# Kernel optimization log

Hardware: AMD Instinct MI355X
Metric: run time of the kernel (lower is better)

Reference implementation:

```python
import jax, jax.numpy as jnp
import numpy as np

B, N, D = 2, 2048, 1024   # batch, seq_len, d_model
E = 2 * D                  # d_inner = d_model * expand_factor
F = 4 * D                  # ffn hidden
CHUNK = 128
EPS_LN = 1e-5


def setup_inputs() -> dict:
    key = jax.random.key(0)
    ks = jax.random.split(key, 16)
    s = 0.02
    return {
        "x": jax.random.normal(ks[0], (B, N, D), dtype=jnp.float32),
        # linear-attention projections (stored [in, out])
        "q_w": jax.random.normal(ks[1], (D, E), dtype=jnp.float32) * s,
        "q_b": jnp.zeros((E,), jnp.float32),
        "k_w": jax.random.normal(ks[2], (D, E), dtype=jnp.float32) * s,
        "k_b": jnp.zeros((E,), jnp.float32),
        "v_w": jax.random.normal(ks[3], (D, E), dtype=jnp.float32) * s,
        "v_b": jnp.zeros((E,), jnp.float32),
        "o_w": jax.random.normal(ks[4], (E, D), dtype=jnp.float32) * s,
        "o_b": jnp.zeros((D,), jnp.float32),
        # layer norms
        "ln1_g": jnp.ones((D,), jnp.float32), "ln1_b": jnp.zeros((D,), jnp.float32),
        "ln2_g": jnp.ones((D,), jnp.float32), "ln2_b": jnp.zeros((D,), jnp.float32),
        # ffn
        "w1": jax.random.normal(ks[5], (D, F), dtype=jnp.float32) * s,
        "b1": jnp.zeros((F,), jnp.float32),
        "w2": jax.random.normal(ks[6], (F, D), dtype=jnp.float32) * s,
        "b2": jnp.zeros((D,), jnp.float32),
    }


def _layer_norm(x, g, b):
    mu = jnp.mean(x, axis=-1, keepdims=True)
    var = jnp.mean(jnp.square(x - mu), axis=-1, keepdims=True)
    return (x - mu) * jax.lax.rsqrt(var + EPS_LN) * g + b


def _feature_map(x):
    return jax.nn.elu(x) + 1.0  # positive features


def _causal_linear_attention(Q, K, V):
    """Exactly cumsum(k v^T) formulation, computed chunk-recurrently.
    Q,K: [B,N,E] (post feature map), V: [B,N,E]. Returns [B,N,E]."""
    nC = N // CHUNK
    Qc = Q.reshape(B, nC, CHUNK, E).transpose(1, 0, 2, 3)
    Kc = K.reshape(B, nC, CHUNK, E).transpose(1, 0, 2, 3)
    Vc = V.reshape(B, nC, CHUNK, E).transpose(1, 0, 2, 3)
    tril = jnp.tril(jnp.ones((CHUNK, CHUNK), Q.dtype))

    def step(S, qkv):  # S: [B,E,E] running sum of k v^T
        q, k, v = qkv
        scores = jnp.einsum('bcd,bkd->bck', q, k) * tril  # intra-chunk causal
        intra = jnp.einsum('bck,bke->bce', scores, v)
        inter = jnp.einsum('bcd,bde->bce', q, S)
        S = S + jnp.einsum('bcd,bce->bde', k, v)
        return S, intra + inter

    S0 = jnp.zeros((B, E, E), Q.dtype)
    _, num = jax.lax.scan(step, S0, (Qc, Kc, Vc))  # [nC,B,CHUNK,E]
    num = num.transpose(1, 0, 2, 3).reshape(B, N, E)
    Z = jnp.cumsum(K, axis=1)                       # [B,N,E]
    den = jnp.einsum('bnd,bnd->bn', Q, Z)[..., None] + 1e-6
    return num / den


def reference(x, q_w, q_b, k_w, k_b, v_w, v_b, o_w, o_b,
              ln1_g, ln1_b, ln2_g, ln2_b, w1, b1, w2, b2):
    # training branch of SSDFLUIDLayer (linear attention), dropout = identity (eval)
    xn = _layer_norm(x, ln1_g, ln1_b)
    Q = _feature_map(xn @ q_w + q_b)
    K = _feature_map(xn @ k_w + k_b)
    V = xn @ v_w + v_b
    attn = _causal_linear_attention(Q, K, V) @ o_w + o_b
    x = x + attn
    xn2 = _layer_norm(x, ln2_g, ln2_b)
    ffn = jax.nn.gelu(xn2 @ w1 + b1, approximate=False) @ w2 + b2
    return x + ffn
```

## Files before the change

kernel.cpp:

```cpp
#include <hip/hip_runtime.h>
#include <math.h>

typedef unsigned short u16;
typedef short s16x8 __attribute__((ext_vector_type(8)));
typedef float f32x4 __attribute__((ext_vector_type(4)));
typedef long long ll;

__device__ inline u16 f2bf(float f) {
    unsigned u = __float_as_uint(f);
    u += 0x7fffu + ((u >> 16) & 1u);
    return (u16)(u >> 16);
}
__device__ inline float bf2f(u16 h) { return __uint_as_float(((unsigned)h) << 16); }

__device__ __forceinline__ void glds16(const u16* g, u16* l) {
    __builtin_amdgcn_global_load_lds(
        (__attribute__((address_space(1))) void*)(void*)g,
        (__attribute__((address_space(3))) void*)l, 16, 0, 0);
}

__global__ __launch_bounds__(256) void ln_bf16(const float* __restrict__ x,
                                               const float* __restrict__ g,
                                               const float* __restrict__ b,
                                               u16* __restrict__ out, int D) {
    int row = blockIdx.x;
    const float* xr = x + (size_t)row * D;
    int t = threadIdx.x;
    float4 v = ((const float4*)xr)[t];
    float s = v.x + v.y + v.z + v.w;
    __shared__ float sm[4];
    #pragma unroll
    for (int o = 32; o > 0; o >>= 1) s += __shfl_down(s, o, 64);
    int lane = t & 63, wv = t >> 6;
    if (lane == 0) sm[wv] = s;
    __syncthreads();
    float mean = (sm[0] + sm[1] + sm[2] + sm[3]) * (1.0f / 1024.0f);
    float dx = v.x - mean, dy = v.y - mean, dz = v.z - mean, dw = v.w - mean;
    float s2 = dx * dx + dy * dy + dz * dz + dw * dw;
    __syncthreads();
    #pragma unroll
    for (int o = 32; o > 0; o >>= 1) s2 += __shfl_down(s2, o, 64);
    if (lane == 0) sm[wv] = s2;
    __syncthreads();
    float var = (sm[0] + sm[1] + sm[2] + sm[3]) * (1.0f / 1024.0f);
    float rstd = rsqrtf(var + 1e-5f);
    float4 gg = ((const float4*)g)[t], bb = ((const float4*)b)[t];
    ushort4 o4;
    o4.x = f2bf(dx * rstd * gg.x + bb.x);
    o4.y = f2bf(dy * rstd * gg.y + bb.y);
    o4.z = f2bf(dz * rstd * gg.z + bb.z);
    o4.w = f2bf(dw * rstd * gg.w + bb.w);
    ((ushort4*)(out + (size_t)row * D))[t] = o4;
}

__global__ __launch_bounds__(256) void combine_ln(
    const float* __restrict__ x, const float* __restrict__ p0,
    const float* __restrict__ p1, const float* __restrict__ ob,
    const float* __restrict__ g, const float* __restrict__ b,
    float* __restrict__ x2, u16* __restrict__ xn2) {
    int row = blockIdx.x;
    int t = threadIdx.x;
    size_t base = (size_t)row * 256;
    float4 v = ((const float4*)x)[base + t];
    float4 a0 = ((const float4*)p0)[base + t];
    float4 a1 = ((const float4*)p1)[base + t];
    float4 ob4 = ((const float4*)ob)[t];
    v.x += a0.x + a1.x + ob4.x;
    v.y += a0.y + a1.y + ob4.y;
    v.z += a0.z + a1.z + ob4.z;
    v.w += a0.w + a1.w + ob4.w;
    ((float4*)x2)[base + t] = v;
    float s = v.x + v.y + v.z + v.w;
    __shared__ float sm[4];
    #pragma unroll
    for (int o = 32; o > 0; o >>= 1) s += __shfl_down(s, o, 64);
    int lane = t & 63, wv = t >> 6;
    if (lane == 0) sm[wv] = s;
    __syncthreads();
    float mean = (sm[0] + sm[1] + sm[2] + sm[3]) * (1.0f / 1024.0f);
    float dx = v.x - mean, dy = v.y - mean, dz = v.z - mean, dw = v.w - mean;
    float s2 = dx * dx + dy * dy + dz * dz + dw * dw;
    __syncthreads();
    #pragma unroll
    for (int o = 32; o > 0; o >>= 1) s2 += __shfl_down(s2, o, 64);
    if (lane == 0) sm[wv] = s2;
    __syncthreads();
    float var = (sm[0] + sm[1] + sm[2] + sm[3]) * (1.0f / 1024.0f);
    float rstd = rsqrtf(var + 1e-5f);
    float4 gg = ((const float4*)g)[t], bb = ((const float4*)b)[t];
    ushort4 o4;
    o4.x = f2bf(dx * rstd * gg.x + bb.x);
    o4.y = f2bf(dy * rstd * gg.y + bb.y);
    o4.z = f2bf(dz * rstd * gg.z + bb.z);
    o4.w = f2bf(dw * rstd * gg.w + bb.w);
    ((ushort4*)(xn2 + (size_t)row * 1024))[t] = o4;
}

__global__ __launch_bounds__(256) void combine_out(
    const float* __restrict__ x2, const float* __restrict__ p0,
    const float* __restrict__ p1, const float* __restrict__ b2,
    float* __restrict__ out) {
    size_t i = (size_t)blockIdx.x * 256 + threadIdx.x;
    int col4 = (int)(i & 255);
    float4 v = ((const float4*)x2)[i];
    float4 a0 = ((const float4*)p0)[i];
    float4 a1 = ((const float4*)p1)[i];
    float4 bb = ((const float4*)b2)[col4];
    v.x += a0.x + a1.x + bb.x;
    v.y += a0.y + a1.y + bb.y;
    v.z += a0.z + a1.z + bb.z;
    v.w += a0.w + a1.w + bb.w;
    ((float4*)out)[i] = v;
}

__global__ void prep(const float* __restrict__ qb, const float* __restrict__ kb,
                     const float* __restrict__ vb, float* __restrict__ bcat,
                     float* __restrict__ den, int E, int BN) {
    int i = blockIdx.x * 256 + threadIdx.x;
    if (i < E) {
        bcat[i] = qb[i];
        bcat[E + i] = kb[i];
        bcat[2 * E + i] = vb[i];
    }
    if (i < BN) den[i] = 0.f;
}

__global__ __launch_bounds__(256) void transpose_all(
    const float* __restrict__ q_w, const float* __restrict__ k_w,
    const float* __restrict__ v_w, const float* __restrict__ o_w,
    const float* __restrict__ w1, const float* __restrict__ w2,
    u16* __restrict__ qkvT, u16* __restrict__ oT,
    u16* __restrict__ w1T, u16* __restrict__ w2T) {
    int z = blockIdx.y;
    const float* src;
    u16* dst;
    int R, C, tprLog;
    switch (z) {
        case 0: src = q_w; dst = qkvT;                           R = 1024; C = 2048; tprLog = 6; break;
        case 1: src = k_w; dst = qkvT + (size_t)2 * 1024 * 1024; R = 1024; C = 2048; tprLog = 6; break;
        case 2: src = v_w; dst = qkvT + (size_t)4 * 1024 * 1024; R = 1024; C = 2048; tprLog = 6; break;
        case 3: src = o_w; dst = oT;                             R = 2048; C = 1024; tprLog = 5; break;
        case 4: src = w1;  dst = w1T;                            R = 1024; C = 4096; tprLog = 7; break;
        default: src = w2; dst = w2T;                            R = 4096; C = 1024; tprLog = 5; break;
    }
    int bx = blockIdx.x;
    int ntiles = (R >> 5) << (tprLog);
    if (bx >= ntiles) return;
    int c0 = (bx & ((1 << tprLog) - 1)) * 32;
    int r0 = (bx >> tprLog) * 32;
    __shared__ u16 tile[32][33];
    int tx = threadIdx.x & 31, ty = threadIdx.x >> 5;
    #pragma unroll
    for (int i = 0; i < 32; i += 8)
        tile[ty + i][tx] = f2bf(src[(size_t)(r0 + ty + i) * C + c0 + tx]);
    __syncthreads();
    #pragma unroll
    for (int i = 0; i < 32; i += 8)
        dst[(size_t)(c0 + ty + i) * R + r0 + tx] = tile[tx][ty + i];
}

__global__ __launch_bounds__(256) void transpose_u16(const u16* __restrict__ in,
                                                     u16* __restrict__ out,
                                                     int R, int C, int ldIn,
                                                     ll sIn, ll sOut) {
    in += (size_t)blockIdx.z * sIn;
    out += (size_t)blockIdx.z * sOut;
    __shared__ u16 tile[32][33];
    int tx = threadIdx.x & 31, ty = threadIdx.x >> 5;
    int c0 = blockIdx.x * 32, r0 = blockIdx.y * 32;
    #pragma unroll
    for (int i = 0; i < 32; i += 8)
        tile[ty + i][tx] = in[(size_t)(r0 + ty + i) * ldIn + c0 + tx];
    __syncthreads();
    #pragma unroll
    for (int i = 0; i < 32; i += 8)
        out[(size_t)(c0 + ty + i) * R + r0 + tx] = tile[tx][ty + i];
}

enum { EPI_QKV = 0, EPI_TRIL = 2, EPI_DIV = 3, EPI_GELU = 5, EPI_PART = 6 };

#define TM 128
#define TN 128

template <int EPI, int BKt>
__global__ __launch_bounds__(256) void gemm_nt(
    const u16* __restrict__ A, const u16* __restrict__ B, void* __restrict__ Cv,
    const float* __restrict__ bias, float* __restrict__ den,
    int M, int N, int K, int lda, int ldb,
    ll sA, ll sB, ll sC, ll sAux) {
    int z = blockIdx.z;
    A += (size_t)z * sA;
    B += (size_t)z * sB;

    int p = blockIdx.y * gridDim.x + blockIdx.x;
    int m0, n0;
    if (EPI == EPI_TRIL || EPI == EPI_DIV) {
        int nb = gridDim.x;
        int panel = nb * 4;
        int pp = p / panel, rr = p - pp * panel;
        m0 = (pp * 4 + (rr & 3)) * TM;
        n0 = (rr >> 2) * TN;
    } else {
        int g = p & 7, r = p >> 3;
        int lw = gridDim.x >> 2, lh = gridDim.y >> 1;
        int ly = r / lw, lx = r - ly * lw;
        m0 = ((g >> 2) * lh + ly) * TM;
        n0 = ((g & 3) * lw + lx) * TN;
    }

    int t = threadIdx.x;

    if (EPI == EPI_TRIL && n0 > m0 + (TM - 1)) {
        u16* C = (u16*)Cv + (size_t)z * sC;
        #pragma unroll
        for (int s = 0; s < 8; ++s) {
            int v = t + 256 * s;
            int row = v >> 4, cf = (v & 15) * 8;
            *(uint4*)&C[(size_t)(m0 + row) * N + n0 + cf] = make_uint4(0, 0, 0, 0);
        }
        return;
    }

    __shared__ __align__(16) u16 As[TM * BKt];
    __shared__ __align__(16) u16 Bs[TN * BKt];

    f32x4 acc[4][4];
    #pragma unroll
    for (int i = 0; i < 4; i++)
        #pragma unroll
        for (int j = 0; j < 4; j++) { f32x4 zz = {0.f, 0.f, 0.f, 0.f}; acc[i][j] = zz; }

    int kend = (EPI == EPI_DIV) ? (m0 + TM < K ? m0 + TM : K) : K;

    int lane = t & 63, wv = t >> 6;
    int lr = lane & 15, q = lane >> 4;
    int wm = (wv & 1) * 64, wn = (wv >> 1) * 64;

    u16* lA = As + wv * 32 * BKt;
    u16* lB = Bs + wv * 32 * BKt;

    int srow, skf;
    if (BKt == 32) {
        srow = wv * 32 + (lane >> 2);
        skf = (((lane & 3) - ((lane >> 3) & 3)) & 3) * 8;
    } else {
        srow = wv * 32 + (lane >> 3);
        skf = (((lane & 7) - (lane >> 3)) & 7) * 8;
    }
    const u16* gA0 = A + (size_t)(m0 + srow) * lda + skf;
    const u16* gB0 = B + (size_t)(n0 + srow) * ldb + skf;

    int ca[2][4], cb[2][4];
    #pragma unroll
    for (int i = 0; i < 4; i++) {
        int ra = wm + i * 16 + lr;
        int rb = wn + i * 16 + lr;
        if (BKt == 32) {
            ca[0][i] = (ra * 4 + ((q + (ra >> 1)) & 3)) * 8;
            cb[0][i] = (rb * 4 + ((q + (rb >> 1)) & 3)) * 8;
        } else {
            ca[0][i] = (ra * 8 + ((q + (ra & 7)) & 7)) * 8;
            ca[1][i] = (ra * 8 + ((4 + q + (ra & 7)) & 7)) * 8;
            cb[0][i] = (rb * 8 + ((q + (rb & 7)) & 7)) * 8;
            cb[1][i] = (rb * 8 + ((4 + q + (rb & 7)) & 7)) * 8;
        }
    }

    for (int k0 = 0; k0 < kend; k0 += BKt) {
        if (BKt == 32) {
            glds16(gA0 + k0, lA);
            glds16(gA0 + k0 + (size_t)16 * lda, lA + 16 * BKt);
            glds16(gB0 + k0, lB);
            glds16(gB0 + k0 + (size_t)16 * ldb, lB + 16 * BKt);
        } else {
            #pragma unroll
            for (int r = 0; r < 4; ++r) {
                glds16(gA0 + k0 + (size_t)(8 * r) * lda, lA + r * 8 * BKt);
                glds16(gB0 + k0 + (size_t)(8 * r) * ldb, lB + r * 8 * BKt);
            }
        }
        __syncthreads();
        #pragma unroll
        for (int kk = 0; kk < BKt / 32; ++kk) {
            s16x8 af[4], bfr[4];
            #pragma unroll
            for (int i = 0; i < 4; i++) af[i] = *(const s16x8*)&As[ca[kk][i]];
            #pragma unroll
            for (int j = 0; j < 4; j++) bfr[j] = *(const s16x8*)&Bs[cb[kk][j]];
            #pragma unroll
            for (int i = 0; i < 4; i++)
                #pragma unroll
                for (int j = 0; j < 4; j++)
                    acc[i][j] = __builtin_amdgcn_mfma_f32_16x16x32_bf16(af[i], bfr[j], acc[i][j], 0, 0, 0);
        }
        __syncthreads();
    }

    u16* Cb = (u16*)Cv + (size_t)z * sC;
    float* Cf = (float*)Cv + (size_t)z * sC;
    bool isQK = (EPI == EPI_QKV) && (n0 < 4096);
    #pragma unroll
    for (int i = 0; i < 4; i++) {
        #pragma unroll
        for (int r = 0; r < 4; r++) {
            int row = m0 + wm + i * 16 + q * 4 + r;
            float rs = 0.f;
            #pragma unroll
            for (int j = 0; j < 4; j++) {
                int col = n0 + wn + j * 16 + lr;
                float v = acc[i][j][r];
                if (EPI == EPI_QKV) {
                    v += bias[col];
                    if (isQK) v = (v > 0.f) ? (v + 1.f) : __expf(v);
                    Cb[(size_t)row * N + col] = f2bf(v);
                } else if (EPI == EPI_TRIL) {
                    v = (col <= row) ? v : 0.f;
                    rs += v;
                    Cb[(size_t)row * N + col] = f2bf(v);
                } else if (EPI == EPI_DIV) {
                    float d = den[(size_t)z * sAux + row] + 1e-6f;
                    Cb[(size_t)row * N + col] = f2bf(v / d);
                } else if (EPI == EPI_GELU) {
                    v += bias[col];
                    float u = v * (0.7978845608f + 0.0356774081f * v * v);
                    u = fminf(u, 40.f);
                    float e = __expf(2.f * u);
                    v = v * __fdividef(e, e + 1.f);
                    Cb[(size_t)row * N + col] = f2bf(v);
                } else if (EPI == EPI_PART) {
                    Cf[(size_t)row * N + col] = v;
                }
            }
            if (EPI == EPI_TRIL) {
                #pragma unroll
                for (int m = 1; m < 16; m <<= 1) rs += __shfl_xor(rs, m, 16);
                if (lr == 0) atomicAdd(&den[(size_t)z * sAux + row], rs);
            }
        }
    }
}

template <int EPI>
__global__ __launch_bounds__(512, 2) void gemm_nt256(
    const u16* __restrict__ A, const u16* __restrict__ B, u16* __restrict__ C,
    const float* __restrict__ bias, int M, int N, int K, int lda, int ldb) {

    __shared__ __align__(16) u16 lds[2][4][128 * 64];

    int p = blockIdx.y * gridDim.x + blockIdx.x;
    int g = p & 7, rr = p >> 3;
    int lw = gridDim.x >> 2, lh = gridDim.y >> 1;
    int ly = rr / lw, lx = rr - ly * lw;
    int m0 = ((g >> 2) * lh + ly) * 256;
    int n0 = ((g & 3) * lw + lx) * 256;

    int t = threadIdx.x;
    int lane = t & 63, wid = t >> 6;
    int lr = lane & 15, q = lane >> 4;

    int sr = wid * 16 + (lane >> 3);
    int skf = (((lane & 7) - (lane >> 3)) & 7) * 8;
    const u16* gA = A + (size_t)(m0 + sr) * lda + skf;
    const u16* gB = B + (size_t)(n0 + sr) * ldb + skf;
    int sd = wid * 1024;

    int nk = K >> 6;

    auto stage = [&](int half, int tt, int d) {
        int kt = tt < nk ? tt : nk - 1;
        const u16* s = (half < 2 ? gA + (size_t)(half * 128) * lda
                                 : gB + (size_t)((half - 2) * 128) * ldb) + kt * 64;
        size_t ld = (half < 2) ? (size_t)lda : (size_t)ldb;
        glds16(s, &lds[d][half][sd]);
        glds16(s + 8 * ld, &lds[d][half][sd + 512]);
    };

    f32x4 acc[8][4];
    #pragma unroll
    for (int i = 0; i < 8; i++)
        #pragma unroll
        for (int j = 0; j < 4; j++) { f32x4 zz = {0.f, 0.f, 0.f, 0.f}; acc[i][j] = zz; }

    int ha = wid >> 2;
    int hb = (wid >> 1) & 1;
    int vb0 = lr * 64 + (((q + lr) & 7) << 3);
    int vb1 = lr * 64 + (((4 + q + lr) & 7) << 3);
    int bb = (wid & 1) * 4096;

    stage(0, 0, 0); stage(1, 0, 0); stage(2, 0, 0); stage(3, 0, 0);
    stage(2, 1, 1); stage(0, 1, 1);
    asm volatile("s_waitcnt vmcnt(4)" ::: "memory");
    asm volatile("s_barrier" ::: "memory");

    s16x8 a[4][2], b0[2][2], b1[2][2];

    for (int tt = 0; tt < nk; ++tt) {
        int cur = tt & 1, nxt = cur ^ 1;
        const u16* Ah = &lds[cur][ha][0];
        const u16* Bh = &lds[cur][2 + hb][bb];

        #pragma unroll
        for (int i = 0; i < 4; i++) {
            a[i][0] = *(const s16x8*)&Ah[vb0 + i * 1024];
            a[i][1] = *(const s16x8*)&Ah[vb1 + i * 1024];
        }
        #pragma unroll
        for (int j = 0; j < 2; j++) {
            b0[j][0] = *(const s16x8*)&Bh[vb0 + j * 1024];
            b0[j][1] = *(const s16x8*)&Bh[vb1 + j * 1024];
        }
        stage(1, tt + 1, nxt);
        asm volatile("s_barrier" ::: "memory");
        asm volatile("s_waitcnt lgkmcnt(0)" ::: "memory");
        __builtin_amdgcn_s_setprio(1);
        #pragma unroll
        for (int i = 0; i < 4; i++)
            #pragma unroll
            for (int j = 0; j < 2; j++) {
                acc[i][j] = __builtin_amdgcn_mfma_f32_16x16x32_bf16(a[i][0], b0[j][0], acc[i][j], 0, 0, 0);
                acc[i][j] = __builtin_amdgcn_mfma_f32_16x16x32_bf16(a[i][1], b0[j][1], acc[i][j], 0, 0, 0);
            }
        __builtin_amdgcn_s_setprio(0);
        asm volatile("s_barrier" ::: "memory");

        #pragma unroll
        for (int j = 0; j < 2; j++) {
            b1[j][0] = *(const s16x8*)&Bh[2048 + vb0 + j * 1024];
            b1[j][1] = *(const s16x8*)&Bh[2048 + vb1 + j * 1024];
        }
        stage(3, tt + 1, nxt);
        asm volatile("s_barrier" ::: "memory");
        asm volatile("s_waitcnt lgkmcnt(0)" ::: "memory");
        __builtin_amdgcn_s_setprio(1);
        #pragma unroll
        for (int i = 0; i < 4; i++)
            #pragma unroll
            for (int j = 0; j < 2; j++) {
                acc[i][2 + j] = __builtin_amdgcn_mfma_f32_16x16x32_bf16(a[i][0], b1[j][0], acc[i][2 + j], 0, 0, 0);
                acc[i][2 + j] = __builtin_amdgcn_mfma_f32_16x16x32_bf16(a[i][1], b1[j][1], acc[i][2 + j], 0, 0, 0);
            }
        __builtin_amdgcn_s_setprio(0);
        asm volatile("s_barrier" ::: "memory");

        #pragma unroll
        for (int i = 0; i < 4; i++) {
            a[i][0] = *(const s16x8*)&Ah[4096 + vb0 + i * 1024];
            a[i][1] = *(const s16x8*)&Ah[4096 + vb1 + i * 1024];
        }
        stage(2, tt + 2, cur);
        asm volatile("s_barrier" ::: "memory");
        asm volatile("s_waitcnt lgkmcnt(0)" ::: "memory");
        __builtin_amdgcn_s_setprio(1);
        #pragma unroll
        for (int i = 0; i < 4; i++)
            #pragma unroll
            for (int j = 0; j < 2; j++) {
                acc[4 + i][2 + j] = __builtin_amdgcn_mfma_f32_16x16x32_bf16(a[i][0], b1[j][0], acc[4 + i][2 + j], 0, 0, 0);
                acc[4 + i][2 + j] = __builtin_amdgcn_mfma_f32_16x16x32_bf16(a[i][1], b1[j][1], acc[4 + i][2 + j], 0, 0, 0);
            }
        __builtin_amdgcn_s_setprio(0);
        asm volatile("s_barrier" ::: "memory");

        stage(0, tt + 2, cur);
        asm volatile("s_barrier" ::: "memory");
        __builtin_amdgcn_s_setprio(1);
        #pragma unroll
        for (int i = 0; i < 4; i++)
            #pragma unroll
            for (int j = 0; j < 2; j++) {
                acc[4 + i][j] = __builtin_amdgcn_mfma_f32_16x16x32_bf16(a[i][0], b0[j][0], acc[4 + i][j], 0, 0, 0);
                acc[4 + i][j] = __builtin_amdgcn_mfma_f32_16x16x32_bf16(a[i][1], b0[j][1], acc[4 + i][j], 0, 0, 0);
            }
        __builtin_amdgcn_s_setprio(0);
        asm volatile("s_waitcnt vmcnt(4)" ::: "memory");
        asm volatile("s_barrier" ::: "memory");
    }

    asm volatile("s_waitcnt vmcnt(0)" ::: "memory");

    int wm = (wid >> 2) * 128, wn = (wid & 3) * 64;
    #pragma unroll
    for (int mi = 0; mi < 8; mi++) {
        #pragma unroll
        for (int r = 0; r < 4; r++) {
            int row = m0 + wm + mi * 16 + q * 4 + r;
            #pragma unroll
            for (int nj = 0; nj < 4; nj++) {
                int col = n0 + wn + nj * 16 + lr;
                float v = acc[mi][nj][r] + bias[col];
                if (EPI == EPI_QKV) {
                    if (n0 + wn + nj * 16 < 4096) v = (v > 0.f) ? (v + 1.f) : __expf(v);
                } else {
                    float u = v * (0.7978845608f + 0.0356774081f * v * v);
                    u = fminf(u, 40.f);
                    float e = __expf(2.f * u);
                    v = v * __fdividef(e, e + 1.f);
                }
                C[(size_t)row * N + col] = f2bf(v);
            }
        }
    }
}

extern "C" void kernel_launch(void* const* d_in, const int* in_sizes, int n_in,
                              void* d_out, int out_size, void* d_ws, size_t ws_size,
                              hipStream_t stream) {
    const float* x    = (const float*)d_in[0];
    const float* q_w  = (const float*)d_in[1];
    const float* q_b  = (const float*)d_in[2];
    const float* k_w  = (const float*)d_in[3];
    const float* k_b  = (const float*)d_in[4];
    const float* v_w  = (const float*)d_in[5];
    const float* v_b  = (const float*)d_in[6];
    const float* o_w  = (const float*)d_in[7];
    const float* o_b  = (const float*)d_in[8];
    const float* ln1g = (const float*)d_in[9];
    const float* ln1b = (const float*)d_in[10];
    const float* ln2g = (const float*)d_in[11];
    const float* ln2b = (const float*)d_in[12];
    const float* w1   = (const float*)d_in[13];
    const float* b1   = (const float*)d_in[14];
    const float* w2   = (const float*)d_in[15];
    const float* b2   = (const float*)d_in[16];
    float* out = (float*)d_out;

    constexpr int Bb = 2, N = 2048, D = 1024, E = 2048, F = 4096;
    constexpr int BN = Bb * N;
    constexpr int E3 = 3 * E;

    char* ws = (char*)d_ws;
    size_t off = 0;
    auto alloc = [&](size_t bytes) -> void* {
        void* p = ws + off;
        off += (bytes + 255) & ~(size_t)255;
        return p;
    };
    u16*   qkvT = (u16*)alloc((size_t)E3 * D * 2);
    u16*   oT   = (u16*)alloc((size_t)D * E * 2);
    u16*   w1T  = (u16*)alloc((size_t)F * D * 2);
    u16*   w2T  = (u16*)alloc((size_t)D * F * 2);
    float* bcat = (float*)alloc((size_t)E3 * 4);
    u16*   xn   = (u16*)alloc((size_t)BN * D * 2);
    u16*   QKV  = (u16*)alloc((size_t)BN * E3 * 2);
    u16*   Vt   = (u16*)alloc((size_t)Bb * E * N * 2);
    u16*   Amat = (u16*)alloc((size_t)Bb * N * N * 2);
    float* den  = (float*)alloc((size_t)BN * 4);

    u16*   xn2 = xn;
    u16*   P   = QKV;
    u16*   h   = QKV + (size_t)8 * 1024 * 1024;
    float* x2  = (float*)Vt;
    float* pt0 = (float*)Amat;
    float* pt1 = pt0 + (size_t)BN * D;

    dim3 blk(256);

    prep<<<dim3((BN + 255) / 256), blk, 0, stream>>>(q_b, k_b, v_b, bcat, den, E, BN);

    transpose_all<<<dim3(4096, 6), blk, 0, stream>>>(
        q_w, k_w, v_w, o_w, w1, w2, qkvT, oT, w1T, w2T);

    ln_bf16<<<BN, blk, 0, stream>>>(x, ln1g, ln1b, xn, D);

    gemm_nt256<EPI_QKV><<<dim3(E3 / 256, BN / 256), dim3(512), 0, stream>>>(
        xn, qkvT, QKV, bcat, BN, E3, D, D, D);

    transpose_u16<<<dim3(E / 32, N / 32, Bb), blk, 0, stream>>>(
        QKV + 2 * E, Vt, N, E, E3, (ll)N * E3, (ll)E * N);

    gemm_nt<EPI_TRIL, 64><<<dim3(N / 128, N / 128, Bb), blk, 0, stream>>>(
        QKV, QKV + E, Amat, nullptr, den, N, N, E, E3, E3,
        (ll)N * E3, (ll)N * E3, (ll)N * N, (ll)N);

    gemm_nt<EPI_DIV, 64><<<dim3(E / 128, N / 128, Bb), blk, 0, stream>>>(
        Amat, Vt, P, nullptr, den, N, E, N, N, N,
        (ll)N * N, (ll)E * N, (ll)N * E, (ll)N);

    gemm_nt<EPI_PART, 64><<<dim3(D / 128, BN / 128, 2), blk, 0, stream>>>(
        P, oT, pt0, nullptr, nullptr, BN, D, E / 2, E, E,
        (ll)(E / 2), (ll)(E / 2), (ll)BN * D, 0);

    combine_ln<<<BN, blk, 0, stream>>>(x, pt0, pt1, o_b, ln2g, ln2b, x2, xn2);

    gemm_nt256<EPI_GELU><<<dim3(F / 256, BN / 256), dim3(512), 0, stream>>>(
        xn2, w1T, h, b1, BN, F, D, D, D);

    gemm_nt<EPI_PART, 64><<<dim3(D / 128, BN / 128, 2), blk, 0, stream>>>(
        h, w2T, pt0, nullptr, nullptr, BN, D, F / 2, F, F,
        (ll)(F / 2), (ll)(F / 2), (ll)BN * D, 0);

    combine_out<<<dim3(BN * D / 4 / 256), blk, 0, stream>>>(x2, pt0, pt1, b2, out);
}
```

Baseline: 458.5 us.

## Add triple-buffered 128x256 GEMM with grouped tile order for QKV projection

Introduces a new bf16 MFMA GEMM kernel with a 128x256 tile, three LDS stages fed by direct global-to-LDS loads, split A/B staging interleaved between two half-tile MFMA phases, and an 8-way grouped block remap for L2 locality. The QKV projection now uses it in place of the 256x256 double-buffered kernel, doubling the grid size. The goal is better latency hiding and more blocks per CU via launch_bounds(512,2), at the cost of a large LDS footprint and a grid remap that assumes the grid dimensions divide evenly.

Result: faster. 446.5 us (-2.6%).

```diff
diff --git a/kernel.cpp b/kernel.cpp
--- a/kernel.cpp
+++ b/kernel.cpp
@@ -502,6 +502,136 @@
     }
 }
 
+template <int EPI>
+__global__ __launch_bounds__(512, 2) void gemm3b(
+    const u16* __restrict__ A, const u16* __restrict__ B, u16* __restrict__ C,
+    const float* __restrict__ bias, int M, int N, int K, int lda, int ldb) {
+
+    __shared__ __align__(16) u16 lds[3][24576];
+
+    int p = blockIdx.y * gridDim.x + blockIdx.x;
+    int g = p & 7, rr = p >> 3;
+    int lw = gridDim.x >> 2, lh = gridDim.y >> 1;
+    int ly = rr / lw, lx = rr - ly * lw;
+    int m0 = ((g >> 2) * lh + ly) * 128;
+    int n0 = ((g & 3) * lw + lx) * 256;
+
+    int t = threadIdx.x;
+    int lane = t & 63, wid = t >> 6;
+    int lr = lane & 15, q = lane >> 4;
+
+    int skf = (((lane & 7) - (lane >> 3)) & 7) * 8;
+    const u16* gA = A + (size_t)(m0 + wid * 16 + (lane >> 3)) * lda + skf;
+    const u16* gB = B + (size_t)(n0 + wid * 32 + (lane >> 3)) * ldb + skf;
+    int sdA = wid * 1024;
+    int sdB = 8192 + wid * 2048;
+
+    int nk = K >> 6;
+
+    auto stageA = [&](int tt, int d) {
+        int kt = (tt < nk ? tt : nk - 1) << 6;
+        glds16(gA + kt, &lds[d][sdA]);
+        glds16(gA + kt + (size_t)8 * lda, &lds[d][sdA + 512]);
+    };
+    auto stageB = [&](int tt, int d) {
+        int kt = (tt < nk ? tt : nk - 1) << 6;
+        #pragma unroll
+        for (int r2 = 0; r2 < 4; ++r2)
+            glds16(gB + kt + (size_t)(8 * r2) * ldb, &lds[d][sdB + r2 * 512]);
+    };
+
+    f32x4 acc[4][4];
+    #pragma unroll
+    for (int i = 0; i < 4; i++)
+        #pragma unroll
+        for (int j = 0; j < 4; j++) { f32x4 zz = {0.f, 0.f, 0.f, 0.f}; acc[i][j] = zz; }
+
+    int wm = (wid >> 2) * 64, wn = (wid & 3) * 64;
+    int aoff0 = wm * 64 + lr * 64 + (((q + lr) & 7) << 3);
+    int aoff1 = wm * 64 + lr * 64 + (((4 + q + lr) & 7) << 3);
+    int boff0 = 8192 + wn * 64 + lr * 64 + (((q + lr) & 7) << 3);
+    int boff1 = 8192 + wn * 64 + lr * 64 + (((4 + q + lr) & 7) << 3);
+
+    stageA(0, 0); stageB(0, 0);
+    stageA(1, 1); stageB(1, 1);
+    asm volatile("s_waitcnt vmcnt(6)" ::: "memory");
+    asm volatile("s_barrier" ::: "memory");
+
+    s16x8 a[4][2], b[4][2];
+
+    for (int tt = 0; tt < nk; ++tt) {
+        int cur = tt % 3, nx2 = (tt + 2) % 3;
+        const u16* L = &lds[cur][0];
+
+        #pragma unroll
+        for (int i = 0; i < 4; i++) {
+            a[i][0] = *(const s16x8*)&L[aoff0 + i * 1024];
+            a[i][1] = *(const s16x8*)&L[aoff1 + i * 1024];
+        }
+        #pragma unroll
+        for (int j = 0; j < 2; j++) {
+            b[j][0] = *(const s16x8*)&L[boff0 + j * 1024];
+            b[j][1] = *(const s16x8*)&L[boff1 + j * 1024];
+        }
+        stageB(tt + 2, nx2);
+        asm volatile("s_barrier" ::: "memory");
+        asm volatile("s_waitcnt lgkmcnt(0)" ::: "memory");
+        __builtin_amdgcn_s_setprio(1);
+        #pragma unroll
+        for (int i = 0; i < 4; i++)
+            #pragma unroll
+            for (int j = 0; j < 2; j++) {
+                acc[i][j] = __builtin_amdgcn_mfma_f32_16x16x32_bf16(a[i][0], b[j][0], acc[i][j], 0, 0, 0);
+                acc[i][j] = __builtin_amdgcn_mfma_f32_16x16x32_bf16(a[i][1], b[j][1], acc[i][j], 0, 0, 0);
+            }
+        __builtin_amdgcn_s_setprio(0);
+        asm volatile("s_barrier" ::: "memory");
+
+        #pragma unroll
+        for (int j = 2; j < 4; j++) {
+            b[j][0] = *(const s16x8*)&L[boff0 + j * 1024];
+            b[j][1] = *(const s16x8*)&L[boff1 + j * 1024];
+        }
+        stageA(tt + 2, nx2);
+        asm volatile("s_barrier" ::: "memory");
+        asm volatile("s_waitcnt lgkmcnt(0)" ::: "memory");
+        __builtin_amdgcn_s_setprio(1);
+        #pragma unroll
+        for (int i = 0; i < 4; i++)
+            #pragma unroll
+            for (int j = 2; j < 4; j++) {
+                acc[i][j] = __builtin_amdgcn_mfma_f32_16x16x32_bf16(a[i][0], b[j][0], acc[i][j], 0, 0, 0);
+                acc[i][j] = __builtin_amdgcn_mfma_f32_16x16x32_bf16(a[i][1], b[j][1], acc[i][j], 0, 0, 0);
+            }
+        __builtin_amdgcn_s_setprio(0);
+        asm volatile("s_waitcnt vmcnt(6)" ::: "memory");
+        asm volatile("s_barrier" ::: "memory");
+    }
+
+    #pragma unroll
+    for (int i = 0; i < 4; i++) {
+        #pragma unroll
+        for (int r = 0; r < 4; r++) {
+            int row = m0 + wm + i * 16 + q * 4 + r;
+            #pragma unroll
+            for (int j = 0; j < 4; j++) {
+                int col = n0 + wn + j * 16 + lr;
+                float v = acc[i][j][r] + bias[col];
+                if (EPI == EPI_QKV) {
+                    if (n0 + wn + j * 16 < 4096) v = (v > 0.f) ? (v + 1.f) : __expf(v);
+                } else {
+                    float u = v * (0.7978845608f + 0.0356774081f * v * v);
+                    u = fminf(u, 40.f);
+                    float e = __expf(2.f * u);
+                    v = v * __fdividef(e, e + 1.f);
+                }
+                C[(size_t)row * N + col] = f2bf(v);
+            }
+        }
+    }
+    asm volatile("s_waitcnt vmcnt(0)" ::: "memory");
+}
+
 extern "C" void kernel_launch(void* const* d_in, const int* in_sizes, int n_in,
                               void* d_out, int out_size, void* d_ws, size_t ws_size,
                               hipStream_t stream) {
@@ -562,7 +692,7 @@
 
     ln_bf16<<<BN, blk, 0, stream>>>(x, ln1g, ln1b, xn, D);
 
-    gemm_nt256<EPI_QKV><<<dim3(E3 / 256, BN / 256), dim3(512), 0, stream>>>(
+    gemm3b<EPI_QKV><<<dim3(E3 / 256, BN / 128), dim3(512), 0, stream>>>(
         xn, qkvT, QKV, bcat, BN, E3, D, D, D);
 
     transpose_u16<<<dim3(E / 32, N / 32, Bb), blk, 0, stream>>>(
```
